# Optimization experiments

Hardware: AMD Instinct MI355X
Metric: run time of the kernel (lower is better)

Reference implementation:

```python
import jax, jax.numpy as jnp
import numpy as np

B, T, D = 64, 256, 1024   # batch, seq_len, input_dim (== hidden_dim)
H = 1024                  # hidden_dim
L = 4                     # layer_dim
O = 512                   # output_dim


def setup_inputs() -> dict:
    key = jax.random.key(0)
    ks = jax.random.split(key, 8)
    s = 1.0 / np.sqrt(H)  # torch LSTMCell default init scale
    u = lambda k, shape: jax.random.uniform(k, shape, jnp.float32, -s, s)
    return {
        "x": jax.random.normal(ks[0], (B, T, D), jnp.float32),
        "W_ih": u(ks[1], (L, 4 * H, D)),   # layer 0 input dim == H
        "W_hh": u(ks[2], (L, 4 * H, H)),
        "b_ih": u(ks[3], (L, 4 * H)),
        "b_hh": u(ks[4], (L, 4 * H)),
        "W_fc": u(ks[5], (O, H)),
        "b_fc": u(ks[6], (O,)),
    }


def _lstm_forward(x, W_ih, W_hh, b_ih, b_hh, W_fc, b_fc):
    def step(carry, x_t):
        h, c = carry  # each [L, B, H]
        inp = x_t     # [B, D]
        for l in range(L):
            gates = inp @ W_ih[l].T + b_ih[l] + h[l] @ W_hh[l].T + b_hh[l]  # [B, 4H]
            i, f, g, o = jnp.split(gates, 4, axis=-1)
            i, f, o = jax.nn.sigmoid(i), jax.nn.sigmoid(f), jax.nn.sigmoid(o)
            g = jnp.tanh(g)
            c_new = f * c[l] + i * g
            h_new = o * jnp.tanh(c_new)
            h = h.at[l].set(h_new)
            c = c.at[l].set(c_new)
            inp = h_new
        return (h, c), None

    h0 = jnp.zeros((L, x.shape[0], H), x.dtype)
    c0 = jnp.zeros((L, x.shape[0], H), x.dtype)
    (h, _), _ = jax.lax.scan(step, (h0, c0), jnp.swapaxes(x, 0, 1))  # scan over time
    return h[-1] @ W_fc.T + b_fc  # [B, O]


def reference(x, W_ih, W_hh, b_ih, b_hh, W_fc, b_fc):
    return _lstm_forward(x, W_ih, W_hh, b_ih, b_hh, W_fc, b_fc)
```

## Files before the change

kernel.cpp:

```cpp
#include <hip/hip_runtime.h>


typedef short           bf16x8 __attribute__((ext_vector_type(8)));
typedef unsigned short  u16x8  __attribute__((ext_vector_type(8)));
typedef float           f32x4  __attribute__((ext_vector_type(4)));

static constexpr int kB  = 64;
static constexpr int kT  = 256;
static constexpr int kH  = 1024;
static constexpr int kL  = 4;
static constexpr int kNG = 4096;
static constexpr int kK2 = 2048;

static constexpr size_t OFF_W    = 0;
static constexpr size_t OFF_BIAS = 67108864;
static constexpr size_t OFF_XB   = 67174400;
static constexpr size_t OFF_H    = 100728832;
static constexpr size_t OFF_C    = 101777408;

static __device__ __forceinline__ unsigned short f2bf(float f) {
  unsigned int u = __float_as_uint(f);
  u += 0x7fffu + ((u >> 16) & 1u);
  return (unsigned short)(u >> 16);
}
static __device__ __forceinline__ float bf2f(unsigned short s) {
  return __uint_as_float(((unsigned int)s) << 16);
}
static __device__ __forceinline__ float sigm_(float x) {
  return 1.0f / (1.0f + __expf(-x));
}
static __device__ __forceinline__ float tanh_(float x) {
  return 1.0f - 2.0f / (__expf(2.0f * x) + 1.0f);
}

__global__ __launch_bounds__(256) void prepack_w(const float* __restrict__ Wih,
                                                 const float* __restrict__ Whh,
                                                 unsigned short* __restrict__ Wcat) {
  const size_t total = (size_t)kL * kNG * kK2;
  for (size_t e = (size_t)blockIdx.x * 256 + threadIdx.x; e < total;
       e += (size_t)gridDim.x * 256) {
    int k = (int)(e & 2047);
    int n = (int)((e >> 11) & 4095);
    int l = (int)(e >> 23);
    int r = (n & 3) * 1024 + (n >> 2);
    float v = (k < 1024) ? Wih[((size_t)l * kNG + r) * 1024 + k]
                         : Whh[((size_t)l * kNG + r) * 1024 + (k - 1024)];
    Wcat[e] = f2bf(v);
  }
}

__global__ __launch_bounds__(256) void prepack_bias(const float* __restrict__ bih,
                                                    const float* __restrict__ bhh,
                                                    float* __restrict__ bias) {
  int e = blockIdx.x * 256 + threadIdx.x;
  int l = e >> 12, n = e & 4095;
  int r = (n & 3) * 1024 + (n >> 2);
  bias[e] = bih[l * kNG + r] + bhh[l * kNG + r];
}

__global__ __launch_bounds__(256) void prepack_x(const float* __restrict__ x,
                                                 unsigned short* __restrict__ xb) {
  size_t e = ((size_t)blockIdx.x * 256 + threadIdx.x) * 8;
  float4 f0 = *(const float4*)(x + e);
  float4 f1 = *(const float4*)(x + e + 4);
  u16x8 v;
  v[0] = f2bf(f0.x); v[1] = f2bf(f0.y); v[2] = f2bf(f0.z); v[3] = f2bf(f0.w);
  v[4] = f2bf(f1.x); v[5] = f2bf(f1.y); v[6] = f2bf(f1.z); v[7] = f2bf(f1.w);
  *(u16x8*)(xb + e) = v;
}

__global__ __launch_bounds__(256) void lstm_diag(
    const unsigned short* __restrict__ Wcat, const float* __restrict__ bias,
    const unsigned short* __restrict__ xb, unsigned short* __restrict__ hbuf,
    float* __restrict__ cbuf, int d) {
  const int l = blockIdx.x >> 6;
  const int t = d - l;
  if (t < 0 || t >= kT) return;
  const int nwg = (blockIdx.x & 63) * 64;

  const int tid  = threadIdx.x;
  const int lane = tid & 63;
  const int w    = tid >> 6;
  const int quad = lane >> 4;
  const int l15  = lane & 15;

  const unsigned short* srcA;
  size_t strideA;
  if (w < 2) {
    if (l == 0) { srcA = xb + (size_t)t * kH + w * 512; strideA = (size_t)kT * kH; }
    else {
      srcA = hbuf + (size_t)((t & 1) * kL + (l - 1)) * (kB * kH) + w * 512;
      strideA = kH;
    }
  } else {
    srcA = hbuf + (size_t)(((t + 1) & 1) * kL + l) * (kB * kH) + (w - 2) * 512;
    strideA = kH;
  }

  const unsigned short* pA[4];
  const unsigned short* pB[4];
  {
    const unsigned short* wrow =
        Wcat + ((size_t)(l * kNG + nwg + l15)) * kK2 + w * 512 + quad * 8;
#pragma unroll
    for (int i = 0; i < 4; ++i) {
      pA[i] = srcA + (size_t)(i * 16 + l15) * strideA + quad * 8;
      pB[i] = wrow + (size_t)i * 16 * kK2;
    }
  }

  f32x4 acc[4][4] = {};
  bf16x8 a0[4], b0[4], a1[4], b1[4];

#pragma unroll
  for (int i = 0; i < 4; ++i) { a0[i] = *(const bf16x8*)(pA[i]); b0[i] = *(const bf16x8*)(pB[i]); }

#pragma unroll
  for (int kc = 0; kc < 16; ++kc) {
    bf16x8* ac = (kc & 1) ? a1 : a0;
    bf16x8* bc = (kc & 1) ? b1 : b0;
    bf16x8* an = (kc & 1) ? a0 : a1;
    bf16x8* bn = (kc & 1) ? b0 : b1;
    if (kc < 15) {
#pragma unroll
      for (int i = 0; i < 4; ++i) {
        an[i] = *(const bf16x8*)(pA[i] + (kc + 1) * 32);
        bn[i] = *(const bf16x8*)(pB[i] + (kc + 1) * 32);
      }
    }
#pragma unroll
    for (int mt = 0; mt < 4; ++mt)
#pragma unroll
      for (int nt = 0; nt < 4; ++nt)
        acc[mt][nt] = __builtin_amdgcn_mfma_f32_16x16x32_bf16(ac[mt], bc[nt],
                                                              acc[mt][nt], 0, 0, 0);
  }

  __shared__ float part[2][64][68];

  if (w >= 2) {
    float* p = &part[w - 2][0][0];
#pragma unroll
    for (int mt = 0; mt < 4; ++mt)
#pragma unroll
      for (int nt = 0; nt < 4; ++nt)
#pragma unroll
        for (int r = 0; r < 4; ++r)
          p[(mt * 16 + quad * 4 + r) * 68 + nt * 16 + l15] = acc[mt][nt][r];
  }
  __syncthreads();
  if (w < 2) {
    const float* p = &part[w][0][0];
#pragma unroll
    for (int mt = 0; mt < 4; ++mt)
#pragma unroll
      for (int nt = 0; nt < 4; ++nt)
#pragma unroll
        for (int r = 0; r < 4; ++r)
          acc[mt][nt][r] += p[(mt * 16 + quad * 4 + r) * 68 + nt * 16 + l15];
  }
  __syncthreads();
  if (w < 2) {
    float* p = &part[w][0][0];
#pragma unroll
    for (int mt = 0; mt < 4; ++mt)
#pragma unroll
      for (int nt = 0; nt < 4; ++nt)
#pragma unroll
        for (int r = 0; r < 4; ++r)
          p[(mt * 16 + quad * 4 + r) * 68 + nt * 16 + l15] = acc[mt][nt][r];
  }
  __syncthreads();

  const int m  = (w << 4) | (lane >> 2);
  const int ug = lane & 3;
  unsigned short* hout = hbuf + (size_t)((t & 1) * kL + l) * (kB * kH);
#pragma unroll
  for (int j = 0; j < 4; ++j) {
    int ul = 4 * j + ug;
    int nb = 4 * ul;
    float4 p0 = *(const float4*)&part[0][m][nb];
    float4 p1 = *(const float4*)&part[1][m][nb];
    float4 bs = *(const float4*)&bias[l * kNG + nwg + nb];
    float gi = sigm_(p0.x + p1.x + bs.x);
    float gf = sigm_(p0.y + p1.y + bs.y);
    float gg = tanh_(p0.z + p1.z + bs.z);
    float go = sigm_(p0.w + p1.w + bs.w);
    int u = (nwg >> 2) + ul;
    size_t ci = ((size_t)l * kB + m) * kH + u;
    float cn = gf * cbuf[ci] + gi * gg;
    cbuf[ci] = cn;
    hout[(size_t)m * kH + u] = f2bf(go * tanh_(cn));
  }
}

__global__ __launch_bounds__(256) void lstm_fc(const unsigned short* __restrict__ h3,
                                               const float* __restrict__ Wfc,
                                               const float* __restrict__ bfc,
                                               float* __restrict__ out) {
  int gt = blockIdx.x * 256 + threadIdx.x;
  int b = gt >> 9, o = gt & 511;
  const unsigned short* hr = h3 + (size_t)b * kH;
  const float* wr = Wfc + (size_t)o * kH;
  float acc = bfc[o];
#pragma unroll 4
  for (int k = 0; k < kH; k += 8) {
    u16x8 hv = *(const u16x8*)(hr + k);
    float4 w0 = *(const float4*)(wr + k);
    float4 w1 = *(const float4*)(wr + k + 4);
    acc += bf2f(hv[0]) * w0.x + bf2f(hv[1]) * w0.y + bf2f(hv[2]) * w0.z +
           bf2f(hv[3]) * w0.w + bf2f(hv[4]) * w1.x + bf2f(hv[5]) * w1.y +
           bf2f(hv[6]) * w1.z + bf2f(hv[7]) * w1.w;
  }
  out[gt] = acc;
}

extern "C" void kernel_launch(void* const* d_in, const int* in_sizes, int n_in,
                              void* d_out, int out_size, void* d_ws, size_t ws_size,
                              hipStream_t stream) {
  (void)in_sizes; (void)n_in; (void)out_size; (void)ws_size;
  const float* x   = (const float*)d_in[0];
  const float* Wih = (const float*)d_in[1];
  const float* Whh = (const float*)d_in[2];
  const float* bih = (const float*)d_in[3];
  const float* bhh = (const float*)d_in[4];
  const float* Wfc = (const float*)d_in[5];
  const float* bfc = (const float*)d_in[6];
  float* out = (float*)d_out;

  char* ws = (char*)d_ws;
  unsigned short* Wcat = (unsigned short*)(ws + OFF_W);
  float*          bias = (float*)(ws + OFF_BIAS);
  unsigned short* xb   = (unsigned short*)(ws + OFF_XB);
  unsigned short* hbuf = (unsigned short*)(ws + OFF_H);
  float*          cbuf = (float*)(ws + OFF_C);

  prepack_w<<<8192, 256, 0, stream>>>(Wih, Whh, Wcat);
  prepack_bias<<<64, 256, 0, stream>>>(bih, bhh, bias);
  prepack_x<<<8192, 256, 0, stream>>>(x, xb);
  hipMemsetAsync(ws + OFF_H, 0, 2097152, stream);

  for (int d = 0; d < kT + kL - 1; ++d)
    lstm_diag<<<256, 256, 0, stream>>>(Wcat, bias, xb, hbuf, cbuf, d);

  lstm_fc<<<128, 256, 0, stream>>>(hbuf + (size_t)7 * kB * kH, Wfc, bfc, out);
}
```

Baseline: 5.960 ms.

## Replace per-diagonal launches with persistent cooperative LSTM kernel using grid sync

```diff
diff --git a/kernel.cpp b/kernel.cpp
--- a/kernel.cpp
+++ b/kernel.cpp
@@ -1,4 +1,7 @@
 #include <hip/hip_runtime.h>
+#include <hip/hip_cooperative_groups.h>
+
+namespace cg = cooperative_groups;
 
 
 typedef short           bf16x8 __attribute__((ext_vector_type(8)));
@@ -10,7 +13,9 @@
 static constexpr int kH  = 1024;
 static constexpr int kL  = 4;
 static constexpr int kNG = 4096;
-static constexpr int kK2 = 2048;
+
+static constexpr int    kABlk   = 65536;
+static constexpr size_t kWLayer = 8388608;
 
 static constexpr size_t OFF_W    = 0;
 static constexpr size_t OFF_BIAS = 67108864;
@@ -35,18 +40,24 @@
 
 __global__ __launch_bounds__(256) void prepack_w(const float* __restrict__ Wih,
                                                  const float* __restrict__ Whh,
-                                                 unsigned short* __restrict__ Wcat) {
-  const size_t total = (size_t)kL * kNG * kK2;
-  for (size_t e = (size_t)blockIdx.x * 256 + threadIdx.x; e < total;
-       e += (size_t)gridDim.x * 256) {
-    int k = (int)(e & 2047);
-    int n = (int)((e >> 11) & 4095);
-    int l = (int)(e >> 23);
-    int r = (n & 3) * 1024 + (n >> 2);
-    float v = (k < 1024) ? Wih[((size_t)l * kNG + r) * 1024 + k]
-                         : Whh[((size_t)l * kNG + r) * 1024 + (k - 1024)];
-    Wcat[e] = f2bf(v);
-  }
+                                                 unsigned short* __restrict__ Wp) {
+  unsigned int e8 = blockIdx.x * 256 + threadIdx.x;
+  const int l15 = e8 & 15;
+  const int k8  = (e8 >> 4) & 255;
+  const int r16 = (e8 >> 12) & 255;
+  const int l   = e8 >> 20;
+  const int n   = r16 * 16 + l15;
+  const int r   = (n & 3) * 1024 + (n >> 2);
+  const int k   = k8 * 8;
+  const float* src = (k < 1024)
+      ? (Wih + ((size_t)l * kNG + r) * 1024 + k)
+      : (Whh + ((size_t)l * kNG + r) * 1024 + (k - 1024));
+  float4 f0 = *(const float4*)(src);
+  float4 f1 = *(const float4*)(src + 4);
+  u16x8 v;
+  v[0] = f2bf(f0.x); v[1] = f2bf(f0.y); v[2] = f2bf(f0.z); v[3] = f2bf(f0.w);
+  v[4] = f2bf(f1.x); v[5] = f2bf(f1.y); v[6] = f2bf(f1.z); v[7] = f2bf(f1.w);
+  *(u16x8*)(Wp + (size_t)e8 * 8) = v;
 }
 
 __global__ __launch_bounds__(256) void prepack_bias(const float* __restrict__ bih,
@@ -59,138 +70,134 @@
 }
 
 __global__ __launch_bounds__(256) void prepack_x(const float* __restrict__ x,
-                                                 unsigned short* __restrict__ xb) {
-  size_t e = ((size_t)blockIdx.x * 256 + threadIdx.x) * 8;
-  float4 f0 = *(const float4*)(x + e);
-  float4 f1 = *(const float4*)(x + e + 4);
+                                                 unsigned short* __restrict__ xp) {
+  unsigned int e8 = blockIdx.x * 256 + threadIdx.x;
+  const int l15 = e8 & 15;
+  const int k8  = (e8 >> 4) & 127;
+  const int m16 = (e8 >> 11) & 3;
+  const int t   = e8 >> 13;
+  const int mm  = m16 * 16 + l15;
+  const float* src = x + ((size_t)mm * kT + t) * kH + k8 * 8;
+  float4 f0 = *(const float4*)(src);
+  float4 f1 = *(const float4*)(src + 4);
   u16x8 v;
   v[0] = f2bf(f0.x); v[1] = f2bf(f0.y); v[2] = f2bf(f0.z); v[3] = f2bf(f0.w);
   v[4] = f2bf(f1.x); v[5] = f2bf(f1.y); v[6] = f2bf(f1.z); v[7] = f2bf(f1.w);
-  *(u16x8*)(xb + e) = v;
-}
-
-__global__ __launch_bounds__(256) void lstm_diag(
-    const unsigned short* __restrict__ Wcat, const float* __restrict__ bias,
-    const unsigned short* __restrict__ xb, unsigned short* __restrict__ hbuf,
-    float* __restrict__ cbuf, int d) {
-  const int l = blockIdx.x >> 6;
-  const int t = d - l;
-  if (t < 0 || t >= kT) return;
-  const int nwg = (blockIdx.x & 63) * 64;
-
+  *(u16x8*)(xp + (size_t)e8 * 8) = v;
+}
+
+__global__ __launch_bounds__(512, 2) void lstm_persist(
+    const unsigned short* __restrict__ Wp, const float* __restrict__ bias,
+    const unsigned short* __restrict__ xp, unsigned short* __restrict__ hp,
+    float* __restrict__ cp) {
+  cg::grid_group grid = cg::this_grid();
+
+  const int l    = blockIdx.x >> 6;
+  const int slab = blockIdx.x & 63;
   const int tid  = threadIdx.x;
   const int lane = tid & 63;
   const int w    = tid >> 6;
   const int quad = lane >> 4;
   const int l15  = lane & 15;
-
-  const unsigned short* srcA;
-  size_t strideA;
-  if (w < 2) {
-    if (l == 0) { srcA = xb + (size_t)t * kH + w * 512; strideA = (size_t)kT * kH; }
-    else {
-      srcA = hbuf + (size_t)((t & 1) * kL + (l - 1)) * (kB * kH) + w * 512;
-      strideA = kH;
+  const int half = w >> 2;
+  const int wloc = w & 3;
+
+  __shared__ float part[8][64][68];
+
+  const unsigned short* pB[4];
+#pragma unroll
+  for (int i = 0; i < 4; ++i)
+    pB[i] = Wp + ((((size_t)(l * 256 + slab * 4 + i)) * 256 +
+                   (size_t)(w * 32 + quad)) * 16 + l15) * 8;
+
+  size_t aoff[4];
+#pragma unroll
+  for (int i = 0; i < 4; ++i)
+    aoff[i] = (((size_t)(i * 128 + wloc * 32 + quad)) * 16 + l15) * 8;
+
+  for (int d = 0; d < kT + kL - 1; ++d) {
+    const int t = d - l;
+    if (t >= 0 && t < kT) {
+      const unsigned short* srcA;
+      if (half == 0) {
+        srcA = (l == 0) ? (xp + (size_t)t * kABlk)
+                        : (hp + ((size_t)((t & 1) * kL + (l - 1))) * kABlk);
+      } else {
+        srcA = hp + ((size_t)(((t + 1) & 1) * kL + l)) * kABlk;
+      }
+
+      f32x4 acc[4][4] = {};
+      bf16x8 Af[3][4], Bw[3][4];
+#pragma unroll
+      for (int i = 0; i < 4; ++i) {
+        Af[0][i] = *(const bf16x8*)(srcA + aoff[i]);
+        Bw[0][i] = *(const bf16x8*)(pB[i]);
+      }
+#pragma unroll
+      for (int i = 0; i < 4; ++i) {
+        Af[1][i] = *(const bf16x8*)(srcA + aoff[i] + 512);
+        Bw[1][i] = *(const bf16x8*)(pB[i] + 512);
+      }
+#pragma unroll
+      for (int kc = 0; kc < 8; ++kc) {
+        const int cur = kc % 3;
+        const int nxt = (kc + 2) % 3;
+        if (kc < 6) {
+#pragma unroll
+          for (int i = 0; i < 4; ++i) {
+            Af[nxt][i] = *(const bf16x8*)(srcA + aoff[i] + (size_t)(kc + 2) * 512);
+            Bw[nxt][i] = *(const bf16x8*)(pB[i] + (size_t)(kc + 2) * 512);
+          }
+        }
+#pragma unroll
+        for (int mt = 0; mt < 4; ++mt)
+#pragma unroll
+          for (int nt = 0; nt < 4; ++nt)
+            acc[mt][nt] = __builtin_amdgcn_mfma_f32_16x16x32_bf16(
+                Af[cur][mt], Bw[cur][nt], acc[mt][nt], 0, 0, 0);
+      }
+
+      {
+        float* p = &part[w][0][0];
+#pragma unroll
+        for (int mt = 0; mt < 4; ++mt)
+#pragma unroll
+          for (int nt = 0; nt < 4; ++nt)
+#pragma unroll
+            for (int r = 0; r < 4; ++r)
+              p[(mt * 16 + quad * 4 + r) * 68 + nt * 16 + l15] = acc[mt][nt][r];
+      }
+      __syncthreads();
+
+      {
+        f32x4 s0 = {}, s1 = {};
+#pragma unroll
+        for (int p8 = 0; p8 < 8; ++p8) {
+          s0 += *(const f32x4*)&part[p8][lane][8 * w];
+          s1 += *(const f32x4*)&part[p8][lane][8 * w + 4];
+        }
+        const float* bb = bias + (size_t)l * kNG + slab * 64 + 8 * w;
+        s0 += *(const f32x4*)bb;
+        s1 += *(const f32x4*)(bb + 4);
+        const int u0 = slab * 16 + 2 * w;
+        const size_t off = ((size_t)((lane >> 4) * 128 + (u0 >> 3))) * 128 +
+                           (lane & 15) * 8 + (u0 & 7);
+        float* cpl = cp + (size_t)l * kABlk + off;
+        float c0 = cpl[0], c1 = cpl[1];
+        float gi0 = sigm_(s0[0]), gf0 = sigm_(s0[1]);
+        float gg0 = tanh_(s0[2]), go0 = sigm_(s0[3]);
+        float gi1 = sigm_(s1[0]), gf1 = sigm_(s1[1]);
+        float gg1 = tanh_(s1[2]), go1 = sigm_(s1[3]);
+        float cn0 = gf0 * c0 + gi0 * gg0;
+        float cn1 = gf1 * c1 + gi1 * gg1;
+        cpl[0] = cn0;
+        cpl[1] = cn1;
+        unsigned int hv = (unsigned int)f2bf(go0 * tanh_(cn0)) |
+                          ((unsigned int)f2bf(go1 * tanh_(cn1)) << 16);
+        *(unsigned int*)(hp + ((size_t)((t & 1) * kL + l)) * kABlk + off) = hv;
+      }
     }
-  } else {
-    srcA = hbuf + (size_t)(((t + 1) & 1) * kL + l) * (kB * kH) + (w - 2) * 512;
-    strideA = kH;
-  }
-
-  const unsigned short* pA[4];
-  const unsigned short* pB[4];
-  {
-    const unsigned short* wrow =
-        Wcat + ((size_t)(l * kNG + nwg + l15)) * kK2 + w * 512 + quad * 8;
-#pragma unroll
-    for (int i = 0; i < 4; ++i) {
-      pA[i] = srcA + (size_t)(i * 16 + l15) * strideA + quad * 8;
-      pB[i] = wrow + (size_t)i * 16 * kK2;
-    }
-  }
-
-  f32x4 acc[4][4] = {};
-  bf16x8 a0[4], b0[4], a1[4], b1[4];
-
-#pragma unroll
-  for (int i = 0; i < 4; ++i) { a0[i] = *(const bf16x8*)(pA[i]); b0[i] = *(const bf16x8*)(pB[i]); }
-
-#pragma unroll
-  for (int kc = 0; kc < 16; ++kc) {
-    bf16x8* ac = (kc & 1) ? a1 : a0;
-    bf16x8* bc = (kc & 1) ? b1 : b0;
-    bf16x8* an = (kc & 1) ? a0 : a1;
-    bf16x8* bn = (kc & 1) ? b0 : b1;
-    if (kc < 15) {
-#pragma unroll
-      for (int i = 0; i < 4; ++i) {
-        an[i] = *(const bf16x8*)(pA[i] + (kc + 1) * 32);
-        bn[i] = *(const bf16x8*)(pB[i] + (kc + 1) * 32);
-      }
-    }
-#pragma unroll
-    for (int mt = 0; mt < 4; ++mt)
-#pragma unroll
-      for (int nt = 0; nt < 4; ++nt)
-        acc[mt][nt] = __builtin_amdgcn_mfma_f32_16x16x32_bf16(ac[mt], bc[nt],
-                                                              acc[mt][nt], 0, 0, 0);
-  }
-
-  __shared__ float part[2][64][68];
-
-  if (w >= 2) {
-    float* p = &part[w - 2][0][0];
-#pragma unroll
-    for (int mt = 0; mt < 4; ++mt)
-#pragma unroll
-      for (int nt = 0; nt < 4; ++nt)
-#pragma unroll
-        for (int r = 0; r < 4; ++r)
-          p[(mt * 16 + quad * 4 + r) * 68 + nt * 16 + l15] = acc[mt][nt][r];
-  }
-  __syncthreads();
-  if (w < 2) {
-    const float* p = &part[w][0][0];
-#pragma unroll
-    for (int mt = 0; mt < 4; ++mt)
-#pragma unroll
-      for (int nt = 0; nt < 4; ++nt)
-#pragma unroll
-        for (int r = 0; r < 4; ++r)
-          acc[mt][nt][r] += p[(mt * 16 + quad * 4 + r) * 68 + nt * 16 + l15];
-  }
-  __syncthreads();
-  if (w < 2) {
-    float* p = &part[w][0][0];
-#pragma unroll
-    for (int mt = 0; mt < 4; ++mt)
-#pragma unroll
-      for (int nt = 0; nt < 4; ++nt)
-#pragma unroll
-        for (int r = 0; r < 4; ++r)
-          p[(mt * 16 + quad * 4 + r) * 68 + nt * 16 + l15] = acc[mt][nt][r];
-  }
-  __syncthreads();
-
-  const int m  = (w << 4) | (lane >> 2);
-  const int ug = lane & 3;
-  unsigned short* hout = hbuf + (size_t)((t & 1) * kL + l) * (kB * kH);
-#pragma unroll
-  for (int j = 0; j < 4; ++j) {
-    int ul = 4 * j + ug;
-    int nb = 4 * ul;
-    float4 p0 = *(const float4*)&part[0][m][nb];
-    float4 p1 = *(const float4*)&part[1][m][nb];
-    float4 bs = *(const float4*)&bias[l * kNG + nwg + nb];
-    float gi = sigm_(p0.x + p1.x + bs.x);
-    float gf = sigm_(p0.y + p1.y + bs.y);
-    float gg = tanh_(p0.z + p1.z + bs.z);
-    float go = sigm_(p0.w + p1.w + bs.w);
-    int u = (nwg >> 2) + ul;
-    size_t ci = ((size_t)l * kB + m) * kH + u;
-    float cn = gf * cbuf[ci] + gi * gg;
-    cbuf[ci] = cn;
-    hout[(size_t)m * kH + u] = f2bf(go * tanh_(cn));
+    grid.sync();
   }
 }
 
@@ -200,14 +207,14 @@
                                                float* __restrict__ out) {
   int gt = blockIdx.x * 256 + threadIdx.x;
   int b = gt >> 9, o = gt & 511;
-  const unsigned short* hr = h3 + (size_t)b * kH;
+  const unsigned short* hr = h3 + (size_t)(b >> 4) * 16384 + (b & 15) * 8;
   const float* wr = Wfc + (size_t)o * kH;
   float acc = bfc[o];
 #pragma unroll 4
-  for (int k = 0; k < kH; k += 8) {
-    u16x8 hv = *(const u16x8*)(hr + k);
-    float4 w0 = *(const float4*)(wr + k);
-    float4 w1 = *(const float4*)(wr + k + 4);
+  for (int k8 = 0; k8 < 128; ++k8) {
+    u16x8 hv = *(const u16x8*)(hr + (size_t)k8 * 128);
+    float4 w0 = *(const float4*)(wr + k8 * 8);
+    float4 w1 = *(const float4*)(wr + k8 * 8 + 4);
     acc += bf2f(hv[0]) * w0.x + bf2f(hv[1]) * w0.y + bf2f(hv[2]) * w0.z +
            bf2f(hv[3]) * w0.w + bf2f(hv[4]) * w1.x + bf2f(hv[5]) * w1.y +
            bf2f(hv[6]) * w1.z + bf2f(hv[7]) * w1.w;
@@ -229,19 +236,20 @@
   float* out = (float*)d_out;
 
   char* ws = (char*)d_ws;
-  unsigned short* Wcat = (unsigned short*)(ws + OFF_W);
+  unsigned short* Wp   = (unsigned short*)(ws + OFF_W);
   float*          bias = (float*)(ws + OFF_BIAS);
-  unsigned short* xb   = (unsigned short*)(ws + OFF_XB);
-  unsigned short* hbuf = (unsigned short*)(ws + OFF_H);
-  float*          cbuf = (float*)(ws + OFF_C);
-
-  prepack_w<<<8192, 256, 0, stream>>>(Wih, Whh, Wcat);
+  unsigned short* xp   = (unsigned short*)(ws + OFF_XB);
+  unsigned short* hpp  = (unsigned short*)(ws + OFF_H);
+  float*          cpp  = (float*)(ws + OFF_C);
+
+  prepack_w<<<16384, 256, 0, stream>>>(Wih, Whh, Wp);
   prepack_bias<<<64, 256, 0, stream>>>(bih, bhh, bias);
-  prepack_x<<<8192, 256, 0, stream>>>(x, xb);
+  prepack_x<<<8192, 256, 0, stream>>>(x, xp);
   hipMemsetAsync(ws + OFF_H, 0, 2097152, stream);
 
-  for (int d = 0; d < kT + kL - 1; ++d)
-    lstm_diag<<<256, 256, 0, stream>>>(Wcat, bias, xb, hbuf, cbuf, d);
-
-  lstm_fc<<<128, 256, 0, stream>>>(hbuf + (size_t)7 * kB * kH, Wfc, bfc, out);
-}
+  void* args[5] = {(void*)&Wp, (void*)&bias, (void*)&xp, (void*)&hpp, (void*)&cpp};
+  hipLaunchCooperativeKernel((void*)lstm_persist, dim3(256), dim3(512), args, 0,
+                             stream);
+
+  lstm_fc<<<128, 256, 0, stream>>>(hpp + (size_t)7 * kABlk, Wfc, bfc, out);
+}
```

Result: slower. 14.03 ms (+135.3%).
